# Kernel tuning notes

Measured on AMD Instinct MI355X. Metric: run time of the kernel, lower is better.

## Reference

```python
import jax, jax.numpy as jnp
import numpy as np
from jax import lax

DIM = 64
K = 3
GROUPS = 1
NUM_KERNELS = 4
B, H, W = 32, 128, 128


def setup_inputs() -> dict:
    key = jax.random.key(0)
    k1, k2, k3, k4 = jax.random.split(key, 4)
    x = jax.random.normal(k1, (B, DIM, H, W), dtype=jnp.float32)
    attention = jax.random.uniform(k2, (B, NUM_KERNELS), dtype=jnp.float32)
    # kaiming-uniform-like init per kernel: bound = sqrt(6 / fan_in)
    fan_in = (DIM // GROUPS) * K * K
    bound = float(np.sqrt(6.0 / fan_in))
    weight = jax.random.uniform(k3, (NUM_KERNELS, DIM, DIM // GROUPS, K, K),
                                dtype=jnp.float32, minval=-bound, maxval=bound)
    bias_p = jax.random.normal(k4, (NUM_KERNELS, DIM), dtype=jnp.float32) * 0.1
    return {"x": x, "attention": attention, "weight": weight, "bias_p": bias_p}


def reference(x, attention, weight, bias_p):
    # Mix kernel bank per sample: [B, nk] @ [nk, dim*dim//g*k*k]
    w_flat = weight.reshape(NUM_KERNELS, -1)
    w_mix = (attention @ w_flat).reshape(B, DIM, DIM // GROUPS, K, K)
    b_mix = attention @ bias_p  # [B, dim]

    def conv_one(xb, wb, bb):
        # xb: [C,H,W], wb: [C_out, C_in//g, k, k]
        out = lax.conv_general_dilated(
            xb[None], wb, window_strides=(1, 1), padding="SAME",
            dimension_numbers=("NCHW", "OIHW", "NCHW"),
            feature_group_count=GROUPS)
        return out[0] + bb[:, None, None]

    return jax.vmap(conv_one)(x, w_mix, b_mix)  # [B, dim, H, W]
```

## Files before the change

### kernel.cpp

```cpp
#include <hip/hip_runtime.h>


#define DIM 64
#define BATCH 32
#define HH 128
#define WW 128
#define NK 4

typedef __attribute__((ext_vector_type(4))) float f32x4;
typedef __attribute__((ext_vector_type(8))) short bf16x8;
typedef __attribute__((ext_vector_type(8))) unsigned short ushort8;

static __device__ __forceinline__ unsigned short f2bf(float f) {
    union { float f; unsigned u; } v; v.f = f;
    unsigned r = v.u + 0x7fffu + ((v.u >> 16) & 1u);
    return (unsigned short)(r >> 16);
}

__global__ __launch_bounds__(256) void mix_weights(
    const float* __restrict__ w, const float* __restrict__ att,
    unsigned short* __restrict__ wmix) {
    __shared__ float tr[4][576];
    int wave = threadIdx.x >> 6, lane = threadIdx.x & 63;
    int idx = blockIdx.x * 4 + wave;
    int b = idx >> 6, co = idx & 63;
    float a[NK];
    #pragma unroll
    for (int k = 0; k < NK; ++k) a[k] = att[b * NK + k];
    float s[9];
    #pragma unroll
    for (int t = 0; t < 9; ++t) s[t] = 0.f;
    #pragma unroll
    for (int k = 0; k < NK; ++k) {
        const float* wp = w + (size_t)(k * DIM + co) * 576;
        #pragma unroll
        for (int t = 0; t < 9; ++t)
            s[t] += a[k] * wp[t * 64 + lane];
    }
    #pragma unroll
    for (int t = 0; t < 9; ++t) tr[wave][t * 64 + lane] = s[t];
    __syncthreads();
    #pragma unroll
    for (int t = 0; t < 9; ++t) {
        float v = tr[wave][lane * 9 + t];
        wmix[(((size_t)b * 9 + t) * DIM + co) * DIM + lane] = f2bf(v);
    }
}

__global__ __launch_bounds__(256) void mix_bias(
    const float* __restrict__ bias, const float* __restrict__ att,
    float* __restrict__ bmix) {
    int idx = blockIdx.x * 256 + threadIdx.x;
    if (idx >= BATCH * DIM) return;
    int b = idx >> 6, co = idx & 63;
    float s = 0.f;
    for (int k = 0; k < NK; ++k) s += att[b * NK + k] * bias[k * DIM + co];
    bmix[idx] = s;
}

__global__ __launch_bounds__(256, 2) void conv_mfma(
    const float* __restrict__ x, const unsigned short* __restrict__ wmix,
    const float* __restrict__ bmix, float* __restrict__ out) {

    __shared__ unsigned short Xs[6 * 66 * 64];
    __shared__ unsigned short Ws[2][64 * 64];

    int bid = blockIdx.x;
    int b   = bid >> 6;
    int r6  = bid & 63;
    int h0  = (r6 >> 1) * 4;
    int w0  = (r6 & 1) * 64;

    int tid  = threadIdx.x;
    int wave = tid >> 6, lane = tid & 63;
    int l15  = lane & 15, q = lane >> 4;

    const int ch0 = tid, ch1 = tid + 256;
    const int co0 = ch0 >> 3, gp0 = ch0 & 7;
    const int co1 = ch1 >> 3, gp1 = ch1 & 7;
    const unsigned short* wsA = wmix + (size_t)b * 9 * 4096 + co0 * 64 + ((gp0 ^ (co0 & 7)) << 3);
    const unsigned short* wsB = wmix + (size_t)b * 9 * 4096 + co1 * 64 + ((gp1 ^ (co1 & 7)) << 3);
    ushort8 wr0 = *(const ushort8*)(wsA);
    ushort8 wr1 = *(const ushort8*)(wsB);

    float biasr[4][4];
    #pragma unroll
    for (int mt = 0; mt < 4; ++mt)
        #pragma unroll
        for (int rg = 0; rg < 4; ++rg)
            biasr[mt][rg] = bmix[b * DIM + mt * 16 + q * 4 + rg];

    #pragma unroll
    for (int half = 0; half < 2; ++half) {
        f32x4 xv[3][4];
        #pragma unroll
        for (int rr = 0; rr < 3; ++rr) {
            int r = half * 3 + rr;
            int hin = h0 - 1 + r;
            bool ok = (hin >= 0) && (hin < HH);
            #pragma unroll
            for (int it = 0; it < 4; ++it) {
                int lin = it * 256 + tid;
                int ci = lin >> 4, c4 = lin & 15;
                f32x4 v = {0.f, 0.f, 0.f, 0.f};
                if (ok)
                    v = *(const f32x4*)&x[(((size_t)b * DIM + ci) * HH + hin) * WW + w0 + c4 * 4];
                xv[rr][it] = v;
            }
        }
        #pragma unroll
        for (int rr = 0; rr < 3; ++rr) {
            int r = half * 3 + rr;
            #pragma unroll
            for (int it = 0; it < 4; ++it) {
                int lin = it * 256 + tid;
                int ci = lin >> 4, c4 = lin & 15;
                #pragma unroll
                for (int j = 0; j < 4; ++j) {
                    int c = c4 * 4 + 1 + j;
                    Xs[(r * 66 + c) * 64 + (((ci >> 3) ^ ((c >> 1) & 7)) << 3) + (ci & 7)] =
                        f2bf(xv[rr][it][j]);
                }
            }
        }
    }
    #pragma unroll
    for (int e = 0; e < 3; ++e) {
        int item = e * 256 + tid;
        int edge = item >= 384;
        int jj = item - edge * 384;
        int ci = jj & 63, r = jj >> 6;
        int hin = h0 - 1 + r;
        int win = edge ? (w0 + 64) : (w0 - 1);
        float v = 0.f;
        if (hin >= 0 && hin < HH && win >= 0 && win < WW)
            v = x[(((size_t)b * DIM + ci) * HH + hin) * WW + win];
        int c = edge ? 65 : 0;
        Xs[(r * 66 + c) * 64 + (((ci >> 3) ^ ((c >> 1) & 7)) << 3) + (ci & 7)] = f2bf(v);
    }

    *(ushort8*)&Ws[0][co0 * 64 + gp0 * 8] = wr0;
    *(ushort8*)&Ws[0][co1 * 64 + gp1 * 8] = wr1;
    wr0 = *(const ushort8*)(wsA + 4096);
    wr1 = *(const ushort8*)(wsB + 4096);

    f32x4 acc[4][4];
    f32x4 zero = {0.f, 0.f, 0.f, 0.f};
    #pragma unroll
    for (int mt = 0; mt < 4; ++mt)
        #pragma unroll
        for (int nt = 0; nt < 4; ++nt) acc[mt][nt] = zero;

    __syncthreads();

    #pragma unroll
    for (int tap = 0; tap < 9; ++tap) {
        int buf = tap & 1;
        if (tap < 8) {
            *(ushort8*)&Ws[buf ^ 1][co0 * 64 + gp0 * 8] = wr0;
            *(ushort8*)&Ws[buf ^ 1][co1 * 64 + gp1 * 8] = wr1;
            if (tap < 7) {
                wr0 = *(const ushort8*)(wsA + (tap + 2) * 4096);
                wr1 = *(const ushort8*)(wsB + (tap + 2) * 4096);
            }
        }
        int kh = tap / 3, kw = tap - kh * 3;
        int r = wave + kh;
        #pragma unroll
        for (int s = 0; s < 2; ++s) {
            int g = s * 4 + q;
            bf16x8 af[4], bfr[4];
            #pragma unroll
            for (int mt = 0; mt < 4; ++mt) {
                int co = mt * 16 + l15;
                af[mt] = *(const bf16x8*)&Ws[buf][co * 64 + ((g ^ (co & 7)) << 3)];
            }
            #pragma unroll
            for (int nt = 0; nt < 4; ++nt) {
                int c = nt * 16 + l15 + kw;
                bfr[nt] = *(const bf16x8*)&Xs[(r * 66 + c) * 64 + ((g ^ ((c >> 1) & 7)) << 3)];
            }
            #pragma unroll
            for (int mt = 0; mt < 4; ++mt)
                #pragma unroll
                for (int nt = 0; nt < 4; ++nt)
                    acc[mt][nt] = __builtin_amdgcn_mfma_f32_16x16x32_bf16(
                        af[mt], bfr[nt], acc[mt][nt], 0, 0, 0);
        }
        __syncthreads();
    }

    int h = h0 + wave;
    #pragma unroll
    for (int mt = 0; mt < 4; ++mt) {
        #pragma unroll
        for (int nt = 0; nt < 4; ++nt) {
            int wcol = w0 + nt * 16 + l15;
            #pragma unroll
            for (int rg = 0; rg < 4; ++rg) {
                int co = mt * 16 + q * 4 + rg;
                out[(((size_t)b * DIM + co) * HH + h) * WW + wcol] = acc[mt][nt][rg] + biasr[mt][rg];
            }
        }
    }
}

extern "C" void kernel_launch(void* const* d_in, const int* in_sizes, int n_in,
                              void* d_out, int out_size, void* d_ws, size_t ws_size,
                              hipStream_t stream) {
    const float* x   = (const float*)d_in[0];
    const float* att = (const float*)d_in[1];
    const float* wgt = (const float*)d_in[2];
    const float* bia = (const float*)d_in[3];
    float* out = (float*)d_out;

    unsigned short* wmix = (unsigned short*)d_ws;
    float* bmix = (float*)((char*)d_ws + 2359296);

    mix_weights<<<512, 256, 0, stream>>>(wgt, att, wmix);
    mix_bias<<<8, 256, 0, stream>>>(bia, att, bmix);
    conv_mfma<<<2048, 256, 0, stream>>>(x, wmix, bmix, out);
}
```

Measured before the change: 261.5 us.

## Halve LDS footprint by staging input channels in two halves; vectorize output stores

```diff
diff --git a/kernel.cpp b/kernel.cpp
--- a/kernel.cpp
+++ b/kernel.cpp
@@ -58,12 +58,15 @@
     bmix[idx] = s;
 }
 
-__global__ __launch_bounds__(256, 2) void conv_mfma(
+#define XIDX(r, c, grp, off) (((r) * 66 + (c)) * 32 + (((grp) ^ (((c) >> 2) & 3)) << 3) + (off))
+#define WIDX(co, grp) ((co) * 32 + (((grp) ^ (((co) >> 1) & 3)) << 3))
+
+__global__ __launch_bounds__(256, 4) void conv_mfma(
     const float* __restrict__ x, const unsigned short* __restrict__ wmix,
     const float* __restrict__ bmix, float* __restrict__ out) {
 
-    __shared__ unsigned short Xs[6 * 66 * 64];
-    __shared__ unsigned short Ws[2][64 * 64];
+    __shared__ unsigned short Xs[6 * 66 * 32];
+    __shared__ unsigned short Ws[2][64 * 32];
 
     int bid = blockIdx.x;
     int b   = bid >> 6;
@@ -75,132 +78,123 @@
     int wave = tid >> 6, lane = tid & 63;
     int l15  = lane & 15, q = lane >> 4;
 
-    const int ch0 = tid, ch1 = tid + 256;
-    const int co0 = ch0 >> 3, gp0 = ch0 & 7;
-    const int co1 = ch1 >> 3, gp1 = ch1 & 7;
-    const unsigned short* wsA = wmix + (size_t)b * 9 * 4096 + co0 * 64 + ((gp0 ^ (co0 & 7)) << 3);
-    const unsigned short* wsB = wmix + (size_t)b * 9 * 4096 + co1 * 64 + ((gp1 ^ (co1 & 7)) << 3);
-    ushort8 wr0 = *(const ushort8*)(wsA);
-    ushort8 wr1 = *(const ushort8*)(wsB);
-
-    float biasr[4][4];
+    const int wco = tid >> 2, wg = tid & 3;
+    const unsigned short* wsrc = wmix + (size_t)b * 9 * 4096 + wco * 64 + wg * 8;
+    const int wdst = WIDX(wco, wg);
+    ushort8 wr = *(const ushort8*)(wsrc);
+
+    float biasr[4];
+    #pragma unroll
+    for (int nt = 0; nt < 4; ++nt) biasr[nt] = bmix[b * DIM + nt * 16 + l15];
+
+    const int P = tid >> 4, c4 = tid & 15;
+    const int xg = P >> 2, xoff = 2 * (P & 3);
+
+    f32x4 acc[4][4];
+    f32x4 zero = {0.f, 0.f, 0.f, 0.f};
     #pragma unroll
     for (int mt = 0; mt < 4; ++mt)
         #pragma unroll
-        for (int rg = 0; rg < 4; ++rg)
-            biasr[mt][rg] = bmix[b * DIM + mt * 16 + q * 4 + rg];
-
-    #pragma unroll
-    for (int half = 0; half < 2; ++half) {
-        f32x4 xv[3][4];
-        #pragma unroll
-        for (int rr = 0; rr < 3; ++rr) {
-            int r = half * 3 + rr;
-            int hin = h0 - 1 + r;
-            bool ok = (hin >= 0) && (hin < HH);
+        for (int nt = 0; nt < 4; ++nt) acc[mt][nt] = zero;
+
+    auto stage_x = [&](int half) {
+        #pragma unroll
+        for (int r2 = 0; r2 < 6; r2 += 2) {
+            f32x4 v[2][2];
             #pragma unroll
-            for (int it = 0; it < 4; ++it) {
-                int lin = it * 256 + tid;
-                int ci = lin >> 4, c4 = lin & 15;
-                f32x4 v = {0.f, 0.f, 0.f, 0.f};
-                if (ok)
-                    v = *(const f32x4*)&x[(((size_t)b * DIM + ci) * HH + hin) * WW + w0 + c4 * 4];
-                xv[rr][it] = v;
-            }
-        }
-        #pragma unroll
-        for (int rr = 0; rr < 3; ++rr) {
-            int r = half * 3 + rr;
+            for (int dr = 0; dr < 2; ++dr) {
+                int r = r2 + dr, hin = h0 - 1 + r;
+                bool ok = (hin >= 0) && (hin < HH);
+                int ci = half * 32 + 2 * P;
+                const float* xp = &x[(((size_t)b * DIM + ci) * HH + hin) * WW + w0 + c4 * 4];
+                v[dr][0] = zero; v[dr][1] = zero;
+                if (ok) { v[dr][0] = *(const f32x4*)xp; v[dr][1] = *(const f32x4*)(xp + HH * WW); }
+            }
             #pragma unroll
-            for (int it = 0; it < 4; ++it) {
-                int lin = it * 256 + tid;
-                int ci = lin >> 4, c4 = lin & 15;
+            for (int dr = 0; dr < 2; ++dr) {
+                int r = r2 + dr;
                 #pragma unroll
                 for (int j = 0; j < 4; ++j) {
                     int c = c4 * 4 + 1 + j;
-                    Xs[(r * 66 + c) * 64 + (((ci >> 3) ^ ((c >> 1) & 7)) << 3) + (ci & 7)] =
-                        f2bf(xv[rr][it][j]);
+                    unsigned pk = (unsigned)f2bf(v[dr][0][j]) |
+                                  ((unsigned)f2bf(v[dr][1][j]) << 16);
+                    *(unsigned*)&Xs[XIDX(r, c, xg, xoff)] = pk;
                 }
             }
         }
-    }
-    #pragma unroll
-    for (int e = 0; e < 3; ++e) {
-        int item = e * 256 + tid;
-        int edge = item >= 384;
-        int jj = item - edge * 384;
-        int ci = jj & 63, r = jj >> 6;
-        int hin = h0 - 1 + r;
-        int win = edge ? (w0 + 64) : (w0 - 1);
-        float v = 0.f;
-        if (hin >= 0 && hin < HH && win >= 0 && win < WW)
-            v = x[(((size_t)b * DIM + ci) * HH + hin) * WW + win];
-        int c = edge ? 65 : 0;
-        Xs[(r * 66 + c) * 64 + (((ci >> 3) ^ ((c >> 1) & 7)) << 3) + (ci & 7)] = f2bf(v);
-    }
-
-    *(ushort8*)&Ws[0][co0 * 64 + gp0 * 8] = wr0;
-    *(ushort8*)&Ws[0][co1 * 64 + gp1 * 8] = wr1;
-    wr0 = *(const ushort8*)(wsA + 4096);
-    wr1 = *(const ushort8*)(wsB + 4096);
-
-    f32x4 acc[4][4];
-    f32x4 zero = {0.f, 0.f, 0.f, 0.f};
-    #pragma unroll
-    for (int mt = 0; mt < 4; ++mt)
-        #pragma unroll
-        for (int nt = 0; nt < 4; ++nt) acc[mt][nt] = zero;
-
+        #pragma unroll
+        for (int e = 0; e < 2; ++e) {
+            int idx = e * 256 + tid;
+            if (idx < 384) {
+                int edge = idx >= 192;
+                int rem  = idx - edge * 192;
+                int ci   = rem & 31, r = rem >> 5;
+                int hin  = h0 - 1 + r;
+                int win  = edge ? (w0 + 64) : (w0 - 1);
+                float vv = 0.f;
+                if (hin >= 0 && hin < HH && win >= 0 && win < WW)
+                    vv = x[(((size_t)b * DIM + half * 32 + ci) * HH + hin) * WW + win];
+                int c = edge ? 65 : 0;
+                Xs[XIDX(r, c, ci >> 3, ci & 7)] = f2bf(vv);
+            }
+        }
+    };
+
+    stage_x(0);
+    *(ushort8*)&Ws[0][wdst] = wr;
+    wr = *(const ushort8*)(wsrc + 4096);
     __syncthreads();
 
     #pragma unroll
-    for (int tap = 0; tap < 9; ++tap) {
-        int buf = tap & 1;
-        if (tap < 8) {
-            *(ushort8*)&Ws[buf ^ 1][co0 * 64 + gp0 * 8] = wr0;
-            *(ushort8*)&Ws[buf ^ 1][co1 * 64 + gp1 * 8] = wr1;
-            if (tap < 7) {
-                wr0 = *(const ushort8*)(wsA + (tap + 2) * 4096);
-                wr1 = *(const ushort8*)(wsB + (tap + 2) * 4096);
-            }
-        }
-        int kh = tap / 3, kw = tap - kh * 3;
-        int r = wave + kh;
-        #pragma unroll
-        for (int s = 0; s < 2; ++s) {
-            int g = s * 4 + q;
-            bf16x8 af[4], bfr[4];
+    for (int t = 0; t < 18; ++t) {
+        const int tap = (t < 9) ? t : t - 9;
+        const int buf = t & 1;
+        if (t < 17) {
+            *(ushort8*)&Ws[buf ^ 1][wdst] = wr;
+            if (t < 16) {
+                int tn = t + 2;
+                int tapn = (tn < 9) ? tn : tn - 9;
+                int halfn = (tn < 9) ? 0 : 1;
+                wr = *(const ushort8*)(wsrc + tapn * 4096 + halfn * 32);
+            }
+        }
+        const int kh = tap / 3, kw = tap - kh * 3;
+        const int r = wave + kh;
+        bf16x8 af[4], bfr[4];
+        #pragma unroll
+        for (int mt = 0; mt < 4; ++mt) {
+            int c = mt * 16 + l15 + kw;
+            af[mt] = *(const bf16x8*)&Xs[XIDX(r, c, q, 0)];
+        }
+        #pragma unroll
+        for (int nt = 0; nt < 4; ++nt) {
+            int co = nt * 16 + l15;
+            bfr[nt] = *(const bf16x8*)&Ws[buf][WIDX(co, q)];
+        }
+        #pragma unroll
+        for (int mt = 0; mt < 4; ++mt)
             #pragma unroll
-            for (int mt = 0; mt < 4; ++mt) {
-                int co = mt * 16 + l15;
-                af[mt] = *(const bf16x8*)&Ws[buf][co * 64 + ((g ^ (co & 7)) << 3)];
-            }
-            #pragma unroll
-            for (int nt = 0; nt < 4; ++nt) {
-                int c = nt * 16 + l15 + kw;
-                bfr[nt] = *(const bf16x8*)&Xs[(r * 66 + c) * 64 + ((g ^ ((c >> 1) & 7)) << 3)];
-            }
-            #pragma unroll
-            for (int mt = 0; mt < 4; ++mt)
-                #pragma unroll
-                for (int nt = 0; nt < 4; ++nt)
-                    acc[mt][nt] = __builtin_amdgcn_mfma_f32_16x16x32_bf16(
-                        af[mt], bfr[nt], acc[mt][nt], 0, 0, 0);
+            for (int nt = 0; nt < 4; ++nt)
+                acc[mt][nt] = __builtin_amdgcn_mfma_f32_16x16x32_bf16(
+                    af[mt], bfr[nt], acc[mt][nt], 0, 0, 0);
+        if (t == 8) {
+            __syncthreads();
+            stage_x(1);
         }
         __syncthreads();
     }
 
     int h = h0 + wave;
     #pragma unroll
-    for (int mt = 0; mt < 4; ++mt) {
-        #pragma unroll
-        for (int nt = 0; nt < 4; ++nt) {
-            int wcol = w0 + nt * 16 + l15;
-            #pragma unroll
-            for (int rg = 0; rg < 4; ++rg) {
-                int co = mt * 16 + q * 4 + rg;
-                out[(((size_t)b * DIM + co) * HH + h) * WW + wcol] = acc[mt][nt][rg] + biasr[mt][rg];
-            }
+    for (int nt = 0; nt < 4; ++nt) {
+        int co = nt * 16 + l15;
+        float* op = &out[(((size_t)b * DIM + co) * HH + h) * WW + w0 + q * 4];
+        #pragma unroll
+        for (int mt = 0; mt < 4; ++mt) {
+            f32x4 vv = acc[mt][nt];
+            vv[0] += biasr[nt]; vv[1] += biasr[nt];
+            vv[2] += biasr[nt]; vv[3] += biasr[nt];
+            *(f32x4*)(op + mt * 16) = vv;
         }
     }
 }
```

Result: slower. 292.8 us (+11.9%).
